# Kernel optimization log

Measured on AMD Instinct MI355X. Metric: run time of the kernel, lower is better.

Reference implementation:

```python
import jax, jax.numpy as jnp
import numpy as np

VOCAB = 50000
EMBED = 256
BATCH = 16384
NUM_SAMPLED = 4096


def _log_uniform_prob(ids):
    # P(c) = (log(c+2) - log(c+1)) / log(V+1), the log-uniform sampler distribution
    ids = ids.astype(jnp.float32)
    return (jnp.log(ids + 2.0) - jnp.log(ids + 1.0)) / jnp.log(VOCAB + 1.0)


def _expected_count(ids, num_sampled):
    # unique log-uniform sampler expected count: 1 - (1 - p)^num_tries, num_tries ~= num_sampled
    p = _log_uniform_prob(ids)
    return -jnp.expm1(num_sampled * jnp.log1p(-p))


def _sigmoid_xent(logits, labels):
    # stable sigmoid cross-entropy: max(x,0) - x*z + log(1 + exp(-|x|))
    return jnp.maximum(logits, 0.0) - logits * labels + jnp.log1p(jnp.exp(-jnp.abs(logits)))


def setup_inputs() -> dict:
    key = jax.random.key(0)
    k1, k2, k3, k4 = jax.random.split(key, 4)
    embedding = jax.random.normal(k1, (BATCH, EMBED), dtype=jnp.float32)
    target_words = jax.random.randint(k2, (BATCH, 1), 0, VOCAB, dtype=jnp.int64 if jax.config.jax_enable_x64 else jnp.int32)
    sampled_ids = jax.random.randint(k3, (NUM_SAMPLED,), 0, VOCAB, dtype=jnp.int64 if jax.config.jax_enable_x64 else jnp.int32)
    # truncated-normal init with stddev 1/sqrt(embed_size), matching TruncatedNormal
    nce_weight = (jax.random.truncated_normal(k4, -2.0, 2.0, (VOCAB, EMBED), dtype=jnp.float32)
                  * (1.0 / EMBED ** 0.5))
    nce_bias = jnp.zeros((VOCAB,), dtype=jnp.float32)
    return {"embedding": embedding, "target_words": target_words,
            "sampled_ids": sampled_ids, "nce_weight": nce_weight, "nce_bias": nce_bias}


def reference(embedding, target_words, sampled_ids, nce_weight, nce_bias):
    num_sampled = sampled_ids.shape[0]
    labels = target_words[:, 0]                       # [B]

    # gather true-class rows and compute true logits (subtract_log_q=True in tf.nn.nce_loss)
    w_true = nce_weight[labels]                       # [B, D]
    true_logits = (jnp.sum(embedding * w_true, axis=-1) + nce_bias[labels]
                   - jnp.log(_expected_count(labels, num_sampled)))          # [B]

    # gather sampled rows and compute sampled logits
    w_samp = nce_weight[sampled_ids]                  # [S, D]
    sampled_logits = (jnp.einsum('bd,sd->bs', embedding, w_samp) + nce_bias[sampled_ids]
                      - jnp.log(_expected_count(sampled_ids, num_sampled)))  # [B, S]

    # sigmoid cross-entropy: true label 1, sampled labels 0; sum per example, mean over batch
    per_example = _sigmoid_xent(true_logits, 1.0) + jnp.sum(_sigmoid_xent(sampled_logits, 0.0), axis=-1)
    return jnp.mean(per_example)
```

## Files before the change

kernel.cpp:

```cpp
#include <hip/hip_runtime.h>
#include <cstdint>
#include <cstddef>

#define VOCAB 50000
#define EMBED 256
#define BATCH 16384
#define NSAMP 4096

typedef float f32x4 __attribute__((ext_vector_type(4)));
typedef int   i32x8 __attribute__((ext_vector_type(8)));


__device__ __forceinline__ float log_expected_count(int id) {
    float idf = (float)id;
    float p = log1pf(1.0f / (idf + 1.0f)) / logf((float)(VOCAB + 1));
    return __logf(-expm1f((float)NSAMP * log1pf(-p)));
}

__device__ __forceinline__ float softplus_f(float x) {
    float v = __expf(-fabsf(x));
    float p = fmaf(v, 0.03215845f, -0.13606275f);
    p = fmaf(v, p, 0.28947478f);
    p = fmaf(v, p, -0.49190896f);
    p = fmaf(v, p, 0.99949556f);
    return fmaxf(x, 0.0f) + v * p;
}

__device__ __forceinline__ int pk4_fp8(float a, float b, float c, float d) {
    int v = __builtin_amdgcn_cvt_pk_fp8_f32(a, b, 0, false);
    v = __builtin_amdgcn_cvt_pk_fp8_f32(c, d, v, true);
    return v;
}



__global__ __launch_bounds__(256) void k_prep(
        const float* __restrict__ E, const int* __restrict__ tgt,
        const int* __restrict__ sids, const float* __restrict__ W,
        const float* __restrict__ bias,
        unsigned char* __restrict__ EF, unsigned char* __restrict__ BF,
        float* __restrict__ badj, double* __restrict__ pTrue)
{
    const int blk = blockIdx.x, tid = threadIdx.x;
    const int wave = tid >> 6, lane = tid & 63;

    if (blk < 1024) {
        float tsum = 0.0f;
        #pragma unroll
        for (int i = 0; i < 4; ++i) {
            int b = (blk * 4 + wave) + 4096 * i;
            int label = tgt[b];
            float4 e  = ((const float4*)(E + (size_t)b * EMBED))[lane];
            float4 wv = ((const float4*)(W + (size_t)label * EMBED))[lane];
            int pk = pk4_fp8(e.x, e.y, e.z, e.w);
            *(int*)(EF + ((b >> 4) * 4096 + (lane >> 3) * 512
                          + (b & 15) * 32 + (lane & 7) * 4)) = pk;
            float d = e.x * wv.x + e.y * wv.y + e.z * wv.z + e.w * wv.w;
            #pragma unroll
            for (int off = 32; off > 0; off >>= 1) d += __shfl_down(d, off, 64);
            if (lane == 0) {
                float tl = d + bias[label] - log_expected_count(label);
                tsum += softplus_f(-tl);
            }
        }
        __shared__ float ts[4];
        if (lane == 0) ts[wave] = tsum;
        __syncthreads();
        if (tid == 0) pTrue[blk] = (double)((ts[0] + ts[1]) + (ts[2] + ts[3]));
    } else {
        #pragma unroll
        for (int i = 0; i < 4; ++i) {
            int task = (blk - 1024) * 256 + tid + 16384 * i;
            int s = task >> 4, p = task & 15;
            int sid = sids[s];
            const float4* wr = (const float4*)(W + (size_t)sid * EMBED + p * 16);
            float4 w0 = wr[0], w1 = wr[1], w2 = wr[2], w3 = wr[3];
            int4 o;
            o.x = pk4_fp8(w0.x * 16.0f, w0.y * 16.0f, w0.z * 16.0f, w0.w * 16.0f);
            o.y = pk4_fp8(w1.x * 16.0f, w1.y * 16.0f, w1.z * 16.0f, w1.w * 16.0f);
            o.z = pk4_fp8(w2.x * 16.0f, w2.y * 16.0f, w2.z * 16.0f, w2.w * 16.0f);
            o.w = pk4_fp8(w3.x * 16.0f, w3.y * 16.0f, w3.z * 16.0f, w3.w * 16.0f);
            *(int4*)(BF + ((s >> 4) * 4096 + (p >> 1) * 512
                           + (s & 15) * 32 + (p & 1) * 16)) = o;
            if (p == 0) badj[s] = bias[sid] - log_expected_count(sid);
        }
    }
}

__global__ __launch_bounds__(256, 2) void k_gemm(
        const unsigned char* __restrict__ EF,
        const unsigned char* __restrict__ BF,
        const float* __restrict__ badj,
        double* __restrict__ pGemm)
{
    const int tid  = threadIdx.x;
    const int wave = tid >> 6;
    const int lane = tid & 63;
    const int wm_g = blockIdx.y * 8 + (wave >> 1) * 4;
    const int wn_g = blockIdx.x * 8 + (wave & 1) * 4;

    i32x8 af[2][4], bf[2][4];
    #pragma unroll
    for (int s = 0; s < 2; ++s) {
        #pragma unroll
        for (int mi = 0; mi < 4; ++mi)
            af[s][mi] = *(const i32x8*)(EF + (size_t)(wm_g + mi) * 4096
                                        + s * 2048 + lane * 32);
        #pragma unroll
        for (int ni = 0; ni < 4; ++ni)
            bf[s][ni] = *(const i32x8*)(BF + (size_t)(wn_g + ni) * 4096
                                        + s * 2048 + lane * 32);
    }

    f32x4 acc[4][4] = {};
    #pragma unroll
    for (int s = 0; s < 2; ++s)
        #pragma unroll
        for (int mi = 0; mi < 4; ++mi)
            #pragma unroll
            for (int ni = 0; ni < 4; ++ni)
                acc[mi][ni] = __builtin_amdgcn_mfma_scale_f32_16x16x128_f8f6f4(
                    af[s][mi], bf[s][ni], acc[mi][ni],
                    0, 0,
                    0, 0x7F7F7F7F,
                    0, 0x7F7F7F7F);

    float lsum = 0.0f;
    const int r16 = lane & 15;
    #pragma unroll
    for (int ni = 0; ni < 4; ++ni) {
        float ba = badj[(wn_g + ni) * 16 + r16];
        #pragma unroll
        for (int mi = 0; mi < 4; ++mi)
            #pragma unroll
            for (int r = 0; r < 4; ++r)
                lsum += softplus_f(fmaf(acc[mi][ni][r], 0.0625f, ba));
    }
    #pragma unroll
    for (int off = 32; off > 0; off >>= 1) lsum += __shfl_down(lsum, off, 64);
    __shared__ float wsum[4];
    if (lane == 0) wsum[wave] = lsum;
    __syncthreads();
    if (tid == 0)
        pGemm[blockIdx.y * gridDim.x + blockIdx.x] =
            (double)((wsum[0] + wsum[1]) + (wsum[2] + wsum[3]));
}

__global__ __launch_bounds__(256) void k_final(
        const double* __restrict__ pTrue, const double* __restrict__ pGemm,
        float* __restrict__ out)
{
    const int tid = threadIdx.x, wave = tid >> 6, lane = tid & 63;
    double s = 0.0;
    for (int i = tid; i < 1024; i += 256) s += pTrue[i];
    for (int i = tid; i < 4096; i += 256) s += pGemm[i];
    #pragma unroll
    for (int off = 32; off > 0; off >>= 1) s += __shfl_down(s, off, 64);
    __shared__ double wsum[4];
    if (lane == 0) wsum[wave] = s;
    __syncthreads();
    if (tid == 0)
        out[0] = (float)(((wsum[0] + wsum[1]) + (wsum[2] + wsum[3]))
                         * (1.0 / (double)BATCH));
}


extern "C" void kernel_launch(void* const* d_in, const int* in_sizes, int n_in,
                              void* d_out, int out_size, void* d_ws, size_t ws_size,
                              hipStream_t stream) {
    const float* emb  = (const float*)d_in[0];
    const int*   tgt  = (const int*)d_in[1];
    const int*   sids = (const int*)d_in[2];
    const float* W    = (const float*)d_in[3];
    const float* bias = (const float*)d_in[4];
    float* out = (float*)d_out;

    char* ws = (char*)d_ws;
    double*        pTrue = (double*)ws;
    double*        pGemm = (double*)(ws + 8192);
    float*         badj  = (float*)(ws + 40960);
    unsigned char* BF    = (unsigned char*)(ws + 57344);
    unsigned char* EF    = (unsigned char*)(ws + 57344 + 1048576);

    hipLaunchKernelGGL(k_prep, dim3(1088), dim3(256), 0, stream,
                       emb, tgt, sids, W, bias, EF, BF, badj, pTrue);
    hipLaunchKernelGGL(k_gemm, dim3(32, 128), dim3(256), 0, stream,
                       EF, BF, badj, pGemm);
    hipLaunchKernelGGL(k_final, dim3(1), dim3(256), 0, stream,
                       pTrue, pGemm, out);
}
```

Baseline: 141.6 us.

## Stage GEMM operand tiles into LDS via direct global-to-LDS loads

The GEMM kernel now copies each block's 32KB A and B fp8 tiles into shared memory with global_load_lds (16-byte per lane), then reads the MFMA fragments from LDS instead of issuing wide direct global loads. The fp8 packing layout in the prep kernel is rearranged into 1024-byte halves so the 16-byte LDS reads line up with the fragment layout. The 1/16 weight scaling moves into the MFMA's B scale exponent (0x7B), which removes the fmaf in the epilogue. This adds 64KB of LDS per block, which may limit occupancy to one block per CU, and the full-load wait leaves no overlap between copy and compute.

```diff
diff --git a/kernel.cpp b/kernel.cpp
--- a/kernel.cpp
+++ b/kernel.cpp
@@ -8,7 +8,11 @@
 #define NSAMP 4096
 
 typedef float f32x4 __attribute__((ext_vector_type(4)));
+typedef int   i32x4 __attribute__((ext_vector_type(4)));
 typedef int   i32x8 __attribute__((ext_vector_type(8)));
+
+typedef __attribute__((address_space(3))) void lds_void_t;
+typedef __attribute__((address_space(1))) void g_void_t;
 
 
 __device__ __forceinline__ float log_expected_count(int id) {
@@ -53,8 +57,10 @@
             float4 e  = ((const float4*)(E + (size_t)b * EMBED))[lane];
             float4 wv = ((const float4*)(W + (size_t)label * EMBED))[lane];
             int pk = pk4_fp8(e.x, e.y, e.z, e.w);
-            *(int*)(EF + ((b >> 4) * 4096 + (lane >> 3) * 512
-                          + (b & 15) * 32 + (lane & 7) * 4)) = pk;
+            *(int*)(EF + ((b >> 4) * 4096 + (lane >> 5) * 2048
+                          + ((lane >> 2) & 1) * 1024
+                          + ((b & 15) + ((lane >> 3) & 3) * 16) * 16
+                          + (lane & 3) * 4)) = pk;
             float d = e.x * wv.x + e.y * wv.y + e.z * wv.z + e.w * wv.w;
             #pragma unroll
             for (int off = 32; off > 0; off >>= 1) d += __shfl_down(d, off, 64);
@@ -80,8 +86,8 @@
             o.y = pk4_fp8(w1.x * 16.0f, w1.y * 16.0f, w1.z * 16.0f, w1.w * 16.0f);
             o.z = pk4_fp8(w2.x * 16.0f, w2.y * 16.0f, w2.z * 16.0f, w2.w * 16.0f);
             o.w = pk4_fp8(w3.x * 16.0f, w3.y * 16.0f, w3.z * 16.0f, w3.w * 16.0f);
-            *(int4*)(BF + ((s >> 4) * 4096 + (p >> 1) * 512
-                           + (s & 15) * 32 + (p & 1) * 16)) = o;
+            *(int4*)(BF + ((s >> 4) * 4096 + (p >> 3) * 2048 + (p & 1) * 1024
+                           + ((s & 15) + ((p >> 1) & 3) * 16) * 16)) = o;
             if (p == 0) badj[s] = bias[sid] - log_expected_count(sid);
         }
     }
@@ -93,23 +99,46 @@
         const float* __restrict__ badj,
         double* __restrict__ pGemm)
 {
+    __shared__ __align__(16) unsigned char As[32768];
+    __shared__ __align__(16) unsigned char Bs[32768];
+
     const int tid  = threadIdx.x;
     const int wave = tid >> 6;
     const int lane = tid & 63;
-    const int wm_g = blockIdx.y * 8 + (wave >> 1) * 4;
-    const int wn_g = blockIdx.x * 8 + (wave & 1) * 4;
+
+    {
+        const unsigned char* gA = EF + (size_t)blockIdx.y * 32768 + wave * 1024 + lane * 16;
+        const unsigned char* gB = BF + (size_t)blockIdx.x * 32768 + wave * 1024 + lane * 16;
+        unsigned char* lA = As + wave * 1024 + lane * 16;
+        unsigned char* lB = Bs + wave * 1024 + lane * 16;
+        #pragma unroll
+        for (int i = 0; i < 8; ++i) {
+            __builtin_amdgcn_global_load_lds((g_void_t*)(gA + i * 4096),
+                                             (lds_void_t*)(lA + i * 4096), 16, 0, 0);
+            __builtin_amdgcn_global_load_lds((g_void_t*)(gB + i * 4096),
+                                             (lds_void_t*)(lB + i * 4096), 16, 0, 0);
+        }
+    }
+    asm volatile("s_waitcnt vmcnt(0)" ::: "memory");
+    __syncthreads();
+
+    const int wm = (wave >> 1) * 4;
+    const int wn = (wave & 1) * 4;
 
     i32x8 af[2][4], bf[2][4];
     #pragma unroll
     for (int s = 0; s < 2; ++s) {
         #pragma unroll
-        for (int mi = 0; mi < 4; ++mi)
-            af[s][mi] = *(const i32x8*)(EF + (size_t)(wm_g + mi) * 4096
-                                        + s * 2048 + lane * 32);
-        #pragma unroll
-        for (int ni = 0; ni < 4; ++ni)
-            bf[s][ni] = *(const i32x8*)(BF + (size_t)(wn_g + ni) * 4096
-                                        + s * 2048 + lane * 32);
+        for (int g = 0; g < 4; ++g) {
+            const unsigned char* pa = As + (wm + g) * 4096 + s * 2048 + lane * 16;
+            i32x4 alo = *(const i32x4*)pa;
+            i32x4 ahi = *(const i32x4*)(pa + 1024);
+            af[s][g] = __builtin_shufflevector(alo, ahi, 0, 1, 2, 3, 4, 5, 6, 7);
+            const unsigned char* pb = Bs + (wn + g) * 4096 + s * 2048 + lane * 16;
+            i32x4 blo = *(const i32x4*)pb;
+            i32x4 bhi = *(const i32x4*)(pb + 1024);
+            bf[s][g] = __builtin_shufflevector(blo, bhi, 0, 1, 2, 3, 4, 5, 6, 7);
+        }
     }
 
     f32x4 acc[4][4] = {};
@@ -123,22 +152,24 @@
                     af[s][mi], bf[s][ni], acc[mi][ni],
                     0, 0,
                     0, 0x7F7F7F7F,
-                    0, 0x7F7F7F7F);
+                    0, 0x7B7B7B7B);
 
     float lsum = 0.0f;
     const int r16 = lane & 15;
+    const int bn0 = blockIdx.x * 128 + (wave & 1) * 64;
     #pragma unroll
     for (int ni = 0; ni < 4; ++ni) {
-        float ba = badj[(wn_g + ni) * 16 + r16];
+        float ba = badj[bn0 + ni * 16 + r16];
         #pragma unroll
         for (int mi = 0; mi < 4; ++mi)
             #pragma unroll
             for (int r = 0; r < 4; ++r)
-                lsum += softplus_f(fmaf(acc[mi][ni][r], 0.0625f, ba));
+                lsum += softplus_f(acc[mi][ni][r] + ba);
     }
     #pragma unroll
     for (int off = 32; off > 0; off >>= 1) lsum += __shfl_down(lsum, off, 64);
-    __shared__ float wsum[4];
+    __syncthreads();
+    float* wsum = (float*)As;
     if (lane == 0) wsum[wave] = lsum;
     __syncthreads();
     if (tid == 0)
@@ -184,7 +215,7 @@
 
     hipLaunchKernelGGL(k_prep, dim3(1088), dim3(256), 0, stream,
                        emb, tgt, sids, W, bias, EF, BF, badj, pTrue);
-    hipLaunchKernelGGL(k_gemm, dim3(32, 128), dim3(256), 0, stream,
+    hipLaunchKernelGGL(k_gemm, dim3(NSAMP / 128, BATCH / 128), dim3(256), 0, stream,
                        EF, BF, badj, pGemm);
     hipLaunchKernelGGL(k_final, dim3(1), dim3(256), 0, stream,
                        pTrue, pGemm, out);
```

New measurement: 148.3 us. 1.05x slower.
